# Performance work log

Hardware: AMD Instinct MI355X
Metric: run time of the kernel (lower is better)

## Reference

```python
import math
import jax, jax.numpy as jnp
import numpy as np

B, C, P, D = 4, 128, 128, 128  # note: C must equal D (see channel-branch einsum)
H = 8
R = D // H
G = 512
LN_EPS = 1e-5
L1_EPS = 1e-6


def layer_norm(x, g, b):
    m = x.mean(-1, keepdims=True)
    v = x.var(-1, keepdims=True)
    return (x - m) * jax.lax.rsqrt(v + LN_EPS) * g + b


def setup_inputs() -> dict:
    key = jax.random.key(0)
    ks = jax.random.split(key, 8)
    return {
        "qz": jax.random.normal(ks[0], (B, C, P, D), jnp.float32),
        "unary": jax.random.normal(ks[1], (B, C, P, D), jnp.float32),
        "time_u_weight": jax.random.normal(ks[2], (B, D, D), jnp.float32) * 0.05,
        "time_v_weight": jax.random.normal(ks[3], (B, D, D), jnp.float32) * 0.05,
        "channel_u_weight": jax.random.normal(ks[4], (B, D, D), jnp.float32) * 0.05,
        "channel_v_weight": jax.random.normal(ks[5], (B, D, D), jnp.float32) * 0.05,
        "topic_binary": jax.random.normal(ks[6], (B, G, D), jnp.float32) * 0.05,
        "ln_gamma": jnp.ones((D,), jnp.float32),
        "ln_beta": jnp.zeros((D,), jnp.float32),
        "w1": jax.random.normal(ks[7], (D, D), jnp.float32) * (1.0 / math.sqrt(D)),
        "b1": jnp.zeros((D,), jnp.float32),
        "w2": jax.random.normal(jax.random.fold_in(key, 99), (D, D), jnp.float32) * (1.0 / math.sqrt(D)),
        "b2": jnp.zeros((D,), jnp.float32),
    }


def reference(qz, unary, time_u_weight, time_v_weight, channel_u_weight,
              channel_v_weight, topic_binary, ln_gamma, ln_beta, w1, b1, w2, b2):
    old = qz
    qzn = layer_norm(qz, ln_gamma, ln_beta)
    scale = 1.0 / math.sqrt(R)

    def batched_linear(x, w):  # x: [B,C,P,D], w: [B,O,D] -> [B,C,P,O]
        return jnp.einsum('bcpd,bod->bcpo', x, w)

    # ---- time attention branch: attend over patches P per (channel, head) ----
    tu = batched_linear(qzn, time_u_weight).reshape(B, C, P, H, R).transpose(0, 1, 3, 2, 4)  # bchpr
    tv = batched_linear(qzn, time_v_weight).reshape(B, C, P, H, R).transpose(0, 1, 3, 2, 4)
    attn_t = jax.nn.softmax(jnp.einsum('bchpr,bchqr->bchpq', tu, tv) * scale, axis=-1)
    m_t = jnp.einsum('bchpq,bcqd->bchpd', attn_t, qzn).mean(axis=2)  # [B,C,P,D]

    # ---- channel attention branch: attend over channels C per (patch, head) ----
    cu = batched_linear(qzn, channel_u_weight).reshape(B, C, P, H, R).transpose(0, 2, 3, 1, 4)  # bphcr
    cv = batched_linear(qzn, channel_v_weight).reshape(B, C, P, H, R).transpose(0, 2, 3, 1, 4)
    attn_c = jax.nn.softmax(jnp.einsum('bphcr,bphdr->bphcd', cu, cv) * scale, axis=-1)
    qz_patch = qzn.transpose(0, 2, 1, 3)  # [B,P,C,D]; requires C == D
    m_c = (attn_c * qz_patch[:, :, None, :, :]).mean(axis=2).transpose(0, 2, 1, 3)  # [B,C,P,D]

    # ---- topic branch: relu + L1 normalize over topics ----
    qg = jnp.maximum(jnp.einsum('bcpd,bgd->bcpg', qzn, topic_binary), 0.0)
    qg = qg / jnp.clip(qg.sum(axis=-1, keepdims=True), L1_EPS, None)
    m_g = jnp.einsum('bcpg,bgd->bcpd', qg, topic_binary)

    x = 0.5 * (unary + m_t + m_c + m_g + old)
    h = layer_norm(x, ln_gamma, ln_beta)
    h = jax.nn.gelu(h @ w1.T + b1, approximate=False) @ w2.T + b2
    return x + h
```

## Files before the change

### kernel.cpp

```cpp
#include <hip/hip_runtime.h>

typedef __attribute__((ext_vector_type(8))) short short8;
typedef __attribute__((ext_vector_type(4))) float f32x4;
typedef unsigned short u16;
typedef unsigned int u32;

#define DEV static __device__ __forceinline__

constexpr long long NEL = 4LL * 128 * 128 * 128;

DEV float us2f(u16 u) { union { u32 i; float f; } x; x.i = (u32)u << 16; return x.f; }
DEV u16 f2us(float f) {
  union { float f; u32 i; } x; x.f = f;
  u32 r = x.i + 0x7fffu + ((x.i >> 16) & 1u);
  return (u16)(r >> 16);
}
DEV u32 pack2(float a, float b) { return (u32)f2us(a) | ((u32)f2us(b) << 16); }
DEV float gelu_f(float x) { return 0.5f * x * (1.0f + erff(x * 0.70710678118654752f)); }

__global__ __launch_bounds__(256) void ln_kernel(const float* __restrict__ xin,
                                                 const float* __restrict__ gw,
                                                 const float* __restrict__ bw,
                                                 u16* __restrict__ out) {
  int wv = threadIdx.x >> 6, lane = threadIdx.x & 63;
  long long row = (long long)blockIdx.x * 4 + wv;
  const float* xr = xin + row * 128;
  float2 v = *(const float2*)(xr + lane * 2);
  float a0 = v.x, a1 = v.y;
  float s = a0 + a1, q = a0 * a0 + a1 * a1;
  #pragma unroll
  for (int off = 32; off >= 1; off >>= 1) { s += __shfl_xor(s, off); q += __shfl_xor(q, off); }
  float m = s * (1.f / 128.f);
  float vv = q * (1.f / 128.f) - m * m;
  float r = rsqrtf(vv + 1e-5f);
  u32* orow = (u32*)(out + row * 128);
  orow[lane] = pack2((a0 - m) * r * gw[lane * 2] + bw[lane * 2],
                     (a1 - m) * r * gw[lane * 2 + 1] + bw[lane * 2 + 1]);
}

__global__ __launch_bounds__(256) void convert_weights(const float* __restrict__ t0, const float* __restrict__ t1,
                                                       const float* __restrict__ t2, const float* __restrict__ t3,
                                                       const float* __restrict__ w1, const float* __restrict__ w2,
                                                       u16* __restrict__ out) {
  long long e = ((long long)blockIdx.x * 256 + threadIdx.x) * 2;
  const float* src; long long off;
  if (e < 262144) {
    int t = (int)(e >> 16);
    src = t == 0 ? t0 : t == 1 ? t1 : t == 2 ? t2 : t3;
    off = e & 65535;
  } else if (e < 278528) { src = w1; off = e - 262144; }
  else { src = w2; off = e - 278528; }
  float2 v = *(const float2*)(src + off);
  *(u32*)(out + e) = pack2(v.x, v.y);
}

template <int EPI>
__global__ __launch_bounds__(256) void gemm128(const u16* __restrict__ A, const u16* __restrict__ W,
                                               int wbatched, const float* __restrict__ bias,
                                               const float* __restrict__ resid,
                                               float* __restrict__ outf, u16* __restrict__ outb) {
  __shared__ u16 AL[64][136];
  __shared__ u16 WL[128][136];
  int rowbase = blockIdx.x * 64;
  int bb = rowbase >> 14;
  const u32* Au = (const u32*)(A + (long long)rowbase * 128);
  const u32* Wu = (const u32*)(W + (wbatched ? (long long)bb * 16384 : 0));
  int tid = threadIdx.x, l = tid & 63, w = tid >> 6;
  for (int idx = tid; idx < 4096; idx += 256)
    *(u32*)&AL[idx >> 6][(idx & 63) * 2] = Au[idx];
  for (int idx = tid; idx < 8192; idx += 256)
    *(u32*)&WL[idx >> 6][(idx & 63) * 2] = Wu[idx];
  __syncthreads();
  f32x4 acc[8];
  #pragma unroll
  for (int cf = 0; cf < 8; ++cf) acc[cf] = (f32x4){0.f, 0.f, 0.f, 0.f};
  int arow = w * 16 + (l & 15);
  int kg = (l >> 4) * 8;
  #pragma unroll
  for (int k = 0; k < 4; ++k) {
    short8 a = *(const short8*)&AL[arow][k * 32 + kg];
    #pragma unroll
    for (int cf = 0; cf < 8; ++cf) {
      short8 b = *(const short8*)&WL[cf * 16 + (l & 15)][k * 32 + kg];
      acc[cf] = __builtin_amdgcn_mfma_f32_16x16x32_bf16(a, b, acc[cf], 0, 0, 0);
    }
  }
  #pragma unroll
  for (int cf = 0; cf < 8; ++cf) {
    int col = cf * 16 + (l & 15);
    float bv = 0.f;
    if (EPI == 2 || EPI == 3) bv = bias[col];
    #pragma unroll
    for (int j = 0; j < 4; ++j) {
      int row = rowbase + w * 16 + (l >> 4) * 4 + j;
      float v = acc[cf][j];
      if (EPI == 2) {
        outb[(long long)row * 128 + col] = f2us(gelu_f(v + bv));
      } else if (EPI == 3) {
        long long o = (long long)row * 128 + col;
        outf[o] = v + bv + resid[o];
      } else if (EPI == 4) {
        outb[(long long)row * 128 + col] = f2us(v);
      } else {
        int b2i = row >> 14, c = (row >> 7) & 127, p = row & 127;
        outb[((long long)(b2i * 128 + p) * 128 + c) * 128 + col] = f2us(v);
      }
    }
  }
}

__global__ __launch_bounds__(256) void time_attn(const u16* __restrict__ tu,
                                                 const u16* __restrict__ tv,
                                                 const u16* __restrict__ qzn16,
                                                 float* __restrict__ accg) {
  __shared__ u16 ZT[128][136];
  __shared__ u16 SP[4][32][136];
  int bc = blockIdx.x;
  const u16* ub = tu + (long long)bc * 16384;
  const u16* vb = tv + (long long)bc * 16384;
  const u32* zb32 = (const u32*)(qzn16 + (long long)bc * 16384);
  int tid = threadIdx.x, l = tid & 63, w = tid >> 6;
  int lo = l & 15, hi = l >> 4;
  int p0 = w * 32;
  for (int idx = tid; idx < 8192; idx += 256) {
    int dp = idx & 63, q = idx >> 6;
    u32 v = zb32[q * 64 + dp];
    ZT[2 * dp][q] = (u16)v;
    ZT[2 * dp + 1][q] = (u16)(v >> 16);
  }
  const short8 z8 = {0, 0, 0, 0, 0, 0, 0, 0};
  const f32x4 z4 = {0.f, 0.f, 0.f, 0.f};
  f32x4 ssum[2][8];
  #pragma unroll
  for (int i = 0; i < 2; ++i)
    #pragma unroll
    for (int cf = 0; cf < 8; ++cf) ssum[i][cf] = z4;
  bool act = hi < 2;
  for (int h = 0; h < 8; ++h) {
    int koff = h * 16 + hi * 8;
    short8 a[2];
    #pragma unroll
    for (int i = 0; i < 2; ++i)
      a[i] = act ? *(const short8*)(ub + (p0 + i * 16 + lo) * 128 + koff) : z8;
    f32x4 s[2][8];
    #pragma unroll
    for (int cf = 0; cf < 8; ++cf) {
      short8 bf = act ? *(const short8*)(vb + (cf * 16 + lo) * 128 + koff) : z8;
      #pragma unroll
      for (int i = 0; i < 2; ++i)
        s[i][cf] = __builtin_amdgcn_mfma_f32_16x16x32_bf16(a[i], bf, z4, 0, 0, 0);
    }
    float mx[2][4], rs[2][4];
    #pragma unroll
    for (int i = 0; i < 2; ++i)
      #pragma unroll
      for (int j = 0; j < 4; ++j) {
        float m = s[i][0][j];
        #pragma unroll
        for (int cf = 1; cf < 8; ++cf) m = fmaxf(m, s[i][cf][j]);
        #pragma unroll
        for (int off = 1; off <= 8; off <<= 1) m = fmaxf(m, __shfl_xor(m, off));
        mx[i][j] = m;
      }
    #pragma unroll
    for (int i = 0; i < 2; ++i)
      #pragma unroll
      for (int cf = 0; cf < 8; ++cf)
        #pragma unroll
        for (int j = 0; j < 4; ++j)
          s[i][cf][j] = __expf((s[i][cf][j] - mx[i][j]) * 0.25f);
    #pragma unroll
    for (int i = 0; i < 2; ++i)
      #pragma unroll
      for (int j = 0; j < 4; ++j) {
        float t = s[i][0][j];
        #pragma unroll
        for (int cf = 1; cf < 8; ++cf) t += s[i][cf][j];
        #pragma unroll
        for (int off = 1; off <= 8; off <<= 1) t += __shfl_xor(t, off);
        rs[i][j] = 1.f / t;
      }
    #pragma unroll
    for (int i = 0; i < 2; ++i)
      #pragma unroll
      for (int cf = 0; cf < 8; ++cf)
        #pragma unroll
        for (int j = 0; j < 4; ++j)
          ssum[i][cf][j] += s[i][cf][j] * rs[i][j];
  }
  #pragma unroll
  for (int i = 0; i < 2; ++i)
    #pragma unroll
    for (int cf = 0; cf < 8; ++cf)
      #pragma unroll
      for (int j = 0; j < 4; ++j)
        SP[w][i * 16 + hi * 4 + j][cf * 16 + lo] = f2us(ssum[i][cf][j]);
  __syncthreads();
  f32x4 acc[2][8];
  #pragma unroll
  for (int i = 0; i < 2; ++i)
    #pragma unroll
    for (int dt = 0; dt < 8; ++dt) acc[i][dt] = z4;
  #pragma unroll
  for (int kk = 0; kk < 4; ++kk) {
    short8 a[2];
    #pragma unroll
    for (int i = 0; i < 2; ++i)
      a[i] = *(const short8*)&SP[w][i * 16 + lo][kk * 32 + hi * 8];
    #pragma unroll
    for (int dt = 0; dt < 8; ++dt) {
      short8 bf = *(const short8*)&ZT[dt * 16 + lo][kk * 32 + hi * 8];
      #pragma unroll
      for (int i = 0; i < 2; ++i)
        acc[i][dt] = __builtin_amdgcn_mfma_f32_16x16x32_bf16(a[i], bf, acc[i][dt], 0, 0, 0);
    }
  }
  float* og = accg + (long long)bc * 16384;
  #pragma unroll
  for (int i = 0; i < 2; ++i)
    #pragma unroll
    for (int dt = 0; dt < 8; ++dt)
      #pragma unroll
      for (int j = 0; j < 4; ++j)
        og[(p0 + i * 16 + hi * 4 + j) * 128 + dt * 16 + lo] = acc[i][dt][j] * 0.125f;
}

__global__ __launch_bounds__(256) void chan_attn(const u16* __restrict__ cuT,
                                                 const u16* __restrict__ cvT,
                                                 const u16* __restrict__ qzn16,
                                                 float* __restrict__ accg) {
  int bp = blockIdx.x;
  int b = bp >> 7, p = bp & 127;
  const u16* ub = cuT + (long long)bp * 16384;
  const u16* vb = cvT + (long long)bp * 16384;
  int tid = threadIdx.x, l = tid & 63, w = tid >> 6;
  int lo = l & 15, hi = l >> 4;
  int c0 = w * 32;
  const short8 z8 = {0, 0, 0, 0, 0, 0, 0, 0};
  const f32x4 z4 = {0.f, 0.f, 0.f, 0.f};
  f32x4 ssum[2][8];
  #pragma unroll
  for (int i = 0; i < 2; ++i)
    #pragma unroll
    for (int cf = 0; cf < 8; ++cf) ssum[i][cf] = z4;
  bool act = hi < 2;
  for (int h = 0; h < 8; ++h) {
    int koff = h * 16 + hi * 8;
    short8 a[2];
    #pragma unroll
    for (int i = 0; i < 2; ++i)
      a[i] = act ? *(const short8*)(ub + (c0 + i * 16 + lo) * 128 + koff) : z8;
    f32x4 s[2][8];
    #pragma unroll
    for (int cf = 0; cf < 8; ++cf) {
      short8 bf = act ? *(const short8*)(vb + (cf * 16 + lo) * 128 + koff) : z8;
      #pragma unroll
      for (int i = 0; i < 2; ++i)
        s[i][cf] = __builtin_amdgcn_mfma_f32_16x16x32_bf16(a[i], bf, z4, 0, 0, 0);
    }
    float mx[2][4], rs[2][4];
    #pragma unroll
    for (int i = 0; i < 2; ++i)
      #pragma unroll
      for (int j = 0; j < 4; ++j) {
        float m = s[i][0][j];
        #pragma unroll
        for (int cf = 1; cf < 8; ++cf) m = fmaxf(m, s[i][cf][j]);
        #pragma unroll
        for (int off = 1; off <= 8; off <<= 1) m = fmaxf(m, __shfl_xor(m, off));
        mx[i][j] = m;
      }
    #pragma unroll
    for (int i = 0; i < 2; ++i)
      #pragma unroll
      for (int cf = 0; cf < 8; ++cf)
        #pragma unroll
        for (int j = 0; j < 4; ++j)
          s[i][cf][j] = __expf((s[i][cf][j] - mx[i][j]) * 0.25f);
    #pragma unroll
    for (int i = 0; i < 2; ++i)
      #pragma unroll
      for (int j = 0; j < 4; ++j) {
        float t = s[i][0][j];
        #pragma unroll
        for (int cf = 1; cf < 8; ++cf) t += s[i][cf][j];
        #pragma unroll
        for (int off = 1; off <= 8; off <<= 1) t += __shfl_xor(t, off);
        rs[i][j] = 1.f / t;
      }
    #pragma unroll
    for (int i = 0; i < 2; ++i)
      #pragma unroll
      for (int cf = 0; cf < 8; ++cf)
        #pragma unroll
        for (int j = 0; j < 4; ++j)
          ssum[i][cf][j] += s[i][cf][j] * rs[i][j];
  }
  const u16* zb = qzn16 + (long long)b * 2097152;
  float* ob = accg + (long long)b * 2097152;
  #pragma unroll
  for (int i = 0; i < 2; ++i)
    #pragma unroll
    for (int cf = 0; cf < 8; ++cf)
      #pragma unroll
      for (int j = 0; j < 4; ++j) {
        int c = c0 + i * 16 + hi * 4 + j;
        int o = cf * 16 + lo;
        long long off = ((long long)c * 128 + p) * 128 + o;
        ob[off] += ssum[i][cf][j] * 0.125f * us2f(zb[off]);
      }
}

__global__ __launch_bounds__(256) void topic_transpose(const float* __restrict__ topic,
                                                       u16* __restrict__ topicB, u16* __restrict__ topicT) {
  __shared__ u16 tile[64][136];
  int b = blockIdx.x >> 3, gc = blockIdx.x & 7;
  const float* tb = topic + (long long)b * 65536;
  u16* tBo = topicB + (long long)b * 65536;
  for (int idx = threadIdx.x; idx < 64 * 64; idx += 256) {
    int g = idx >> 6, d2 = idx & 63;
    const float2 v = *(const float2*)(tb + (long long)(gc * 64 + g) * 128 + d2 * 2);
    u32 pv = pack2(v.x, v.y);
    *(u32*)&tile[g][d2 * 2] = pv;
    *(u32*)(tBo + (long long)(gc * 64 + g) * 128 + d2 * 2) = pv;
  }
  __syncthreads();
  u16* to = topicT + (long long)b * 65536;
  for (int idx = threadIdx.x; idx < 128 * 64; idx += 256) {
    int d = idx >> 6, g = idx & 63;
    to[d * 512 + gc * 64 + g] = tile[g][d];
  }
}

__global__ __launch_bounds__(256) void topic_kernel(const u16* __restrict__ qzn16,
                                                    const u16* __restrict__ topicB,
                                                    const u16* __restrict__ topicT,
                                                    float* __restrict__ accg) {
  __shared__ u16 AL[32][136];
  __shared__ u16 QG[32][520];
  __shared__ float redsum[4][32];
  int rowbase = blockIdx.x * 32;
  int b = rowbase >> 14;
  const u16* tB = topicB + (long long)b * 65536;
  const u16* tT = topicT + (long long)b * 65536;
  int tid = threadIdx.x, l = tid & 63, w = tid >> 6;
  int lo = l & 15, hi = l >> 4;
  const u32* asrc = (const u32*)(qzn16 + (long long)rowbase * 128);
  for (int idx = tid; idx < 2048; idx += 256)
    *(u32*)&AL[idx >> 6][(idx & 63) * 2] = asrc[idx];
  __syncthreads();
  const f32x4 z4 = {0.f, 0.f, 0.f, 0.f};
  float rsum[2][4] = {{0.f,0.f,0.f,0.f},{0.f,0.f,0.f,0.f}};
  #pragma unroll
  for (int gc = 0; gc < 8; ++gc) {
    f32x4 pa[2] = {z4, z4};
    #pragma unroll
    for (int k = 0; k < 4; ++k) {
      short8 bb = *(const short8*)(tB + (long long)(gc * 64 + w * 16 + lo) * 128 + k * 32 + hi * 8);
      #pragma unroll
      for (int i = 0; i < 2; ++i) {
        short8 a = *(const short8*)&AL[i * 16 + lo][k * 32 + hi * 8];
        pa[i] = __builtin_amdgcn_mfma_f32_16x16x32_bf16(a, bb, pa[i], 0, 0, 0);
      }
    }
    #pragma unroll
    for (int i = 0; i < 2; ++i)
      #pragma unroll
      for (int j = 0; j < 4; ++j) {
        float v = fmaxf(pa[i][j], 0.f);
        QG[i * 16 + hi * 4 + j][gc * 64 + w * 16 + lo] = f2us(v);
        rsum[i][j] += v;
      }
  }
  #pragma unroll
  for (int i = 0; i < 2; ++i)
    #pragma unroll
    for (int j = 0; j < 4; ++j) {
      float t = rsum[i][j];
      #pragma unroll
      for (int off = 1; off <= 8; off <<= 1) t += __shfl_xor(t, off);
      rsum[i][j] = t;
    }
  if (lo == 0) {
    #pragma unroll
    for (int i = 0; i < 2; ++i)
      #pragma unroll
      for (int j = 0; j < 4; ++j)
        redsum[w][i * 16 + hi * 4 + j] = rsum[i][j];
  }
  __syncthreads();
  float inv[2][4];
  #pragma unroll
  for (int i = 0; i < 2; ++i)
    #pragma unroll
    for (int j = 0; j < 4; ++j) {
      int row = i * 16 + hi * 4 + j;
      float s = redsum[0][row] + redsum[1][row] + redsum[2][row] + redsum[3][row];
      inv[i][j] = 1.f / fmaxf(s, 1e-6f);
    }
  f32x4 ba[2][2] = {{z4, z4}, {z4, z4}};
  #pragma unroll
  for (int kc = 0; kc < 16; ++kc) {
    short8 a[2];
    #pragma unroll
    for (int i = 0; i < 2; ++i)
      a[i] = *(const short8*)&QG[i * 16 + lo][kc * 32 + hi * 8];
    #pragma unroll
    for (int cf = 0; cf < 2; ++cf) {
      short8 bb = *(const short8*)(tT + (long long)(w * 32 + cf * 16 + lo) * 512 + kc * 32 + hi * 8);
      #pragma unroll
      for (int i = 0; i < 2; ++i)
        ba[i][cf] = __builtin_amdgcn_mfma_f32_16x16x32_bf16(a[i], bb, ba[i][cf], 0, 0, 0);
    }
  }
  #pragma unroll
  for (int i = 0; i < 2; ++i)
    #pragma unroll
    for (int cf = 0; cf < 2; ++cf)
      #pragma unroll
      for (int j = 0; j < 4; ++j) {
        long long o = (long long)(rowbase + i * 16 + hi * 4 + j) * 128 + w * 32 + cf * 16 + lo;
        accg[o] += ba[i][cf][j] * inv[i][j];
      }
}

__global__ __launch_bounds__(256) void combine_kernel(const float* __restrict__ qz, const float* __restrict__ un,
                                                      float* __restrict__ acc) {
  long long i = ((long long)blockIdx.x * 256 + threadIdx.x) * 4;
  float4 q = *(const float4*)(qz + i);
  float4 u = *(const float4*)(un + i);
  float4 a = *(const float4*)(acc + i);
  float4 r;
  r.x = 0.5f * (q.x + u.x + a.x);
  r.y = 0.5f * (q.y + u.y + a.y);
  r.z = 0.5f * (q.z + u.z + a.z);
  r.w = 0.5f * (q.w + u.w + a.w);
  *(float4*)(acc + i) = r;
}

extern "C" void kernel_launch(void* const* d_in, const int* in_sizes, int n_in,
                              void* d_out, int out_size, void* d_ws, size_t ws_size,
                              hipStream_t stream) {
  const float* qz    = (const float*)d_in[0];
  const float* unary = (const float*)d_in[1];
  const float* tuw   = (const float*)d_in[2];
  const float* tvw   = (const float*)d_in[3];
  const float* cuw   = (const float*)d_in[4];
  const float* cvw   = (const float*)d_in[5];
  const float* topic = (const float*)d_in[6];
  const float* gam   = (const float*)d_in[7];
  const float* bet   = (const float*)d_in[8];
  const float* w1    = (const float*)d_in[9];
  const float* b1    = (const float*)d_in[10];
  const float* w2    = (const float*)d_in[11];
  const float* b2    = (const float*)d_in[12];
  float* out = (float*)d_out;

  char* base = (char*)d_ws;
  u16*   qzn16  = (u16*)base;
  float* accb   = (float*)(base + NEL * 2);
  u16*   bufU16 = (u16*)(base + NEL * 6);
  u16*   bufV16 = (u16*)(base + NEL * 8);
  u16*   wbf    = (u16*)(base + NEL * 10);
  u16*   topicB = wbf + 294912;
  u16*   topicT = topicB + 262144;

  convert_weights<<<576, 256, 0, stream>>>(tuw, tvw, cuw, cvw, w1, w2, wbf);
  topic_transpose<<<32, 256, 0, stream>>>(topic, topicB, topicT);
  ln_kernel<<<16384, 256, 0, stream>>>(qz, gam, bet, qzn16);
  gemm128<4><<<1024, 256, 0, stream>>>(qzn16, wbf,         1, nullptr, nullptr, nullptr, bufU16);
  gemm128<4><<<1024, 256, 0, stream>>>(qzn16, wbf + 65536, 1, nullptr, nullptr, nullptr, bufV16);
  time_attn<<<512, 256, 0, stream>>>(bufU16, bufV16, qzn16, accb);
  gemm128<5><<<1024, 256, 0, stream>>>(qzn16, wbf + 131072, 1, nullptr, nullptr, nullptr, bufU16);
  gemm128<5><<<1024, 256, 0, stream>>>(qzn16, wbf + 196608, 1, nullptr, nullptr, nullptr, bufV16);
  chan_attn<<<512, 256, 0, stream>>>(bufU16, bufV16, qzn16, accb);
  topic_kernel<<<2048, 256, 0, stream>>>(qzn16, topicB, topicT, accb);
  combine_kernel<<<8192, 256, 0, stream>>>(qz, unary, accb);
  ln_kernel<<<16384, 256, 0, stream>>>(accb, gam, bet, bufU16);
  gemm128<2><<<1024, 256, 0, stream>>>(bufU16, wbf + 262144, 0, b1, nullptr, nullptr, bufV16);
  gemm128<3><<<1024, 256, 0, stream>>>(bufV16, wbf + 278528, 0, b2, accb, out, nullptr);
}
```

Baseline: 395.7 us.

## Fuse dual projection GEMMs, stage V in LDS, fold combine+LN into topic kernel

Merges each pair of U/V projection GEMMs into one kernel that loads the activation tile once and reuses it for both weight matrices. The time and channel attention kernels now stage the V tile in shared memory instead of reading it repeatedly from global memory; time_attn reuses that buffer for the softmax scratch. The topic kernel now also does the residual combine and the second layer norm, which removes the separate combine and LN launches and their full-tensor round trips. The fused LN computes variance as E[x^2]-m^2, which is less numerically stable, and the extra shared memory may lower occupancy.

Result: no change. 394.3 us (-0.4%).

```diff
diff --git a/kernel.cpp b/kernel.cpp
--- a/kernel.cpp
+++ b/kernel.cpp
@@ -56,15 +56,14 @@
 
 template <int EPI>
 __global__ __launch_bounds__(256) void gemm128(const u16* __restrict__ A, const u16* __restrict__ W,
-                                               int wbatched, const float* __restrict__ bias,
+                                               const float* __restrict__ bias,
                                                const float* __restrict__ resid,
                                                float* __restrict__ outf, u16* __restrict__ outb) {
   __shared__ u16 AL[64][136];
   __shared__ u16 WL[128][136];
   int rowbase = blockIdx.x * 64;
-  int bb = rowbase >> 14;
   const u32* Au = (const u32*)(A + (long long)rowbase * 128);
-  const u32* Wu = (const u32*)(W + (wbatched ? (long long)bb * 16384 : 0));
+  const u32* Wu = (const u32*)W;
   int tid = threadIdx.x, l = tid & 63, w = tid >> 6;
   for (int idx = tid; idx < 4096; idx += 256)
     *(u32*)&AL[idx >> 6][(idx & 63) * 2] = Au[idx];
@@ -88,24 +87,70 @@
   #pragma unroll
   for (int cf = 0; cf < 8; ++cf) {
     int col = cf * 16 + (l & 15);
-    float bv = 0.f;
-    if (EPI == 2 || EPI == 3) bv = bias[col];
+    float bv = bias[col];
     #pragma unroll
     for (int j = 0; j < 4; ++j) {
       int row = rowbase + w * 16 + (l >> 4) * 4 + j;
       float v = acc[cf][j];
       if (EPI == 2) {
         outb[(long long)row * 128 + col] = f2us(gelu_f(v + bv));
-      } else if (EPI == 3) {
+      } else {
         long long o = (long long)row * 128 + col;
         outf[o] = v + bv + resid[o];
-      } else if (EPI == 4) {
-        outb[(long long)row * 128 + col] = f2us(v);
-      } else {
-        int b2i = row >> 14, c = (row >> 7) & 127, p = row & 127;
-        outb[((long long)(b2i * 128 + p) * 128 + c) * 128 + col] = f2us(v);
-      }
-    }
+      }
+    }
+  }
+}
+
+template <int EPI>
+__global__ __launch_bounds__(256) void gemm_dual(const u16* __restrict__ A,
+                                                 const u16* __restrict__ W0, const u16* __restrict__ W1,
+                                                 u16* __restrict__ out0, u16* __restrict__ out1) {
+  __shared__ u16 AL[64][136];
+  __shared__ u16 WL[128][136];
+  int rowbase = blockIdx.x * 64;
+  int bb = rowbase >> 14;
+  const u32* Au = (const u32*)(A + (long long)rowbase * 128);
+  int tid = threadIdx.x, l = tid & 63, w = tid >> 6;
+  for (int idx = tid; idx < 4096; idx += 256)
+    *(u32*)&AL[idx >> 6][(idx & 63) * 2] = Au[idx];
+  int arow = w * 16 + (l & 15);
+  int kg = (l >> 4) * 8;
+  #pragma unroll
+  for (int widx = 0; widx < 2; ++widx) {
+    const u32* Wu = (const u32*)((widx ? W1 : W0) + (long long)bb * 16384);
+    for (int idx = tid; idx < 8192; idx += 256)
+      *(u32*)&WL[idx >> 6][(idx & 63) * 2] = Wu[idx];
+    __syncthreads();
+    f32x4 acc[8];
+    #pragma unroll
+    for (int cf = 0; cf < 8; ++cf) acc[cf] = (f32x4){0.f, 0.f, 0.f, 0.f};
+    #pragma unroll
+    for (int k = 0; k < 4; ++k) {
+      short8 a = *(const short8*)&AL[arow][k * 32 + kg];
+      #pragma unroll
+      for (int cf = 0; cf < 8; ++cf) {
+        short8 b = *(const short8*)&WL[cf * 16 + (l & 15)][k * 32 + kg];
+        acc[cf] = __builtin_amdgcn_mfma_f32_16x16x32_bf16(a, b, acc[cf], 0, 0, 0);
+      }
+    }
+    u16* ob = widx ? out1 : out0;
+    #pragma unroll
+    for (int cf = 0; cf < 8; ++cf) {
+      int col = cf * 16 + (l & 15);
+      #pragma unroll
+      for (int j = 0; j < 4; ++j) {
+        int row = rowbase + w * 16 + (l >> 4) * 4 + j;
+        float v = acc[cf][j];
+        if (EPI == 4) {
+          ob[(long long)row * 128 + col] = f2us(v);
+        } else {
+          int b2i = row >> 14, c = (row >> 7) & 127, p = row & 127;
+          ob[((long long)(b2i * 128 + p) * 128 + c) * 128 + col] = f2us(v);
+        }
+      }
+    }
+    __syncthreads();
   }
 }
 
@@ -114,20 +159,25 @@
                                                  const u16* __restrict__ qzn16,
                                                  float* __restrict__ accg) {
   __shared__ u16 ZT[128][136];
-  __shared__ u16 SP[4][32][136];
+  __shared__ u16 UB[17408];
+  #define VB_(r, c) UB[(r) * 136 + (c)]
+  #define SP_(wv, r, c) UB[((wv) * 32 + (r)) * 136 + (c)]
   int bc = blockIdx.x;
   const u16* ub = tu + (long long)bc * 16384;
-  const u16* vb = tv + (long long)bc * 16384;
+  const u32* vb32 = (const u32*)(tv + (long long)bc * 16384);
   const u32* zb32 = (const u32*)(qzn16 + (long long)bc * 16384);
   int tid = threadIdx.x, l = tid & 63, w = tid >> 6;
   int lo = l & 15, hi = l >> 4;
   int p0 = w * 32;
   for (int idx = tid; idx < 8192; idx += 256) {
     int dp = idx & 63, q = idx >> 6;
-    u32 v = zb32[q * 64 + dp];
+    u32 v = zb32[idx];
     ZT[2 * dp][q] = (u16)v;
     ZT[2 * dp + 1][q] = (u16)(v >> 16);
   }
+  for (int idx = tid; idx < 8192; idx += 256)
+    *(u32*)&VB_(idx >> 6, (idx & 63) * 2) = vb32[idx];
+  __syncthreads();
   const short8 z8 = {0, 0, 0, 0, 0, 0, 0, 0};
   const f32x4 z4 = {0.f, 0.f, 0.f, 0.f};
   f32x4 ssum[2][8];
@@ -145,7 +195,7 @@
     f32x4 s[2][8];
     #pragma unroll
     for (int cf = 0; cf < 8; ++cf) {
-      short8 bf = act ? *(const short8*)(vb + (cf * 16 + lo) * 128 + koff) : z8;
+      short8 bf = act ? *(const short8*)&VB_(cf * 16 + lo, koff) : z8;
       #pragma unroll
       for (int i = 0; i < 2; ++i)
         s[i][cf] = __builtin_amdgcn_mfma_f32_16x16x32_bf16(a[i], bf, z4, 0, 0, 0);
@@ -188,13 +238,14 @@
         for (int j = 0; j < 4; ++j)
           ssum[i][cf][j] += s[i][cf][j] * rs[i][j];
   }
+  __syncthreads();
   #pragma unroll
   for (int i = 0; i < 2; ++i)
     #pragma unroll
     for (int cf = 0; cf < 8; ++cf)
       #pragma unroll
       for (int j = 0; j < 4; ++j)
-        SP[w][i * 16 + hi * 4 + j][cf * 16 + lo] = f2us(ssum[i][cf][j]);
+        SP_(w, i * 16 + hi * 4 + j, cf * 16 + lo) = f2us(ssum[i][cf][j]);
   __syncthreads();
   f32x4 acc[2][8];
   #pragma unroll
@@ -206,7 +257,7 @@
     short8 a[2];
     #pragma unroll
     for (int i = 0; i < 2; ++i)
-      a[i] = *(const short8*)&SP[w][i * 16 + lo][kk * 32 + hi * 8];
+      a[i] = *(const short8*)&SP_(w, i * 16 + lo, kk * 32 + hi * 8);
     #pragma unroll
     for (int dt = 0; dt < 8; ++dt) {
       short8 bf = *(const short8*)&ZT[dt * 16 + lo][kk * 32 + hi * 8];
@@ -223,19 +274,25 @@
       #pragma unroll
       for (int j = 0; j < 4; ++j)
         og[(p0 + i * 16 + hi * 4 + j) * 128 + dt * 16 + lo] = acc[i][dt][j] * 0.125f;
+  #undef VB_
+  #undef SP_
 }
 
 __global__ __launch_bounds__(256) void chan_attn(const u16* __restrict__ cuT,
                                                  const u16* __restrict__ cvT,
                                                  const u16* __restrict__ qzn16,
                                                  float* __restrict__ accg) {
+  __shared__ u16 VB[128][136];
   int bp = blockIdx.x;
   int b = bp >> 7, p = bp & 127;
   const u16* ub = cuT + (long long)bp * 16384;
-  const u16* vb = cvT + (long long)bp * 16384;
+  const u32* vb32 = (const u32*)(cvT + (long long)bp * 16384);
   int tid = threadIdx.x, l = tid & 63, w = tid >> 6;
   int lo = l & 15, hi = l >> 4;
   int c0 = w * 32;
+  for (int idx = tid; idx < 8192; idx += 256)
+    *(u32*)&VB[idx >> 6][(idx & 63) * 2] = vb32[idx];
+  __syncthreads();
   const short8 z8 = {0, 0, 0, 0, 0, 0, 0, 0};
   const f32x4 z4 = {0.f, 0.f, 0.f, 0.f};
   f32x4 ssum[2][8];
@@ -253,7 +310,7 @@
     f32x4 s[2][8];
     #pragma unroll
     for (int cf = 0; cf < 8; ++cf) {
-      short8 bf = act ? *(const short8*)(vb + (cf * 16 + lo) * 128 + koff) : z8;
+      short8 bf = act ? *(const short8*)&VB[cf * 16 + lo][koff] : z8;
       #pragma unroll
       for (int i = 0; i < 2; ++i)
         s[i][cf] = __builtin_amdgcn_mfma_f32_16x16x32_bf16(a[i], bf, z4, 0, 0, 0);
@@ -332,13 +389,20 @@
   }
 }
 
-__global__ __launch_bounds__(256) void topic_kernel(const u16* __restrict__ qzn16,
-                                                    const u16* __restrict__ topicB,
-                                                    const u16* __restrict__ topicT,
-                                                    float* __restrict__ accg) {
+__global__ __launch_bounds__(256) void topic_fuse(const u16* __restrict__ qzn16,
+                                                  const u16* __restrict__ topicB,
+                                                  const u16* __restrict__ topicT,
+                                                  const float* __restrict__ qz,
+                                                  const float* __restrict__ un,
+                                                  const float* __restrict__ gam,
+                                                  const float* __restrict__ bet,
+                                                  float* __restrict__ accg,
+                                                  u16* __restrict__ xln) {
   __shared__ u16 AL[32][136];
   __shared__ u16 QG[32][520];
-  __shared__ float redsum[4][32];
+  __shared__ float redL[4][32];
+  __shared__ float redS[4][32];
+  __shared__ float redQ[4][32];
   int rowbase = blockIdx.x * 32;
   int b = rowbase >> 14;
   const u16* tB = topicB + (long long)b * 65536;
@@ -350,7 +414,7 @@
     *(u32*)&AL[idx >> 6][(idx & 63) * 2] = asrc[idx];
   __syncthreads();
   const f32x4 z4 = {0.f, 0.f, 0.f, 0.f};
-  float rsum[2][4] = {{0.f,0.f,0.f,0.f},{0.f,0.f,0.f,0.f}};
+  float rsum[2][4] = {{0.f, 0.f, 0.f, 0.f}, {0.f, 0.f, 0.f, 0.f}};
   #pragma unroll
   for (int gc = 0; gc < 8; ++gc) {
     f32x4 pa[2] = {z4, z4};
@@ -386,7 +450,7 @@
     for (int i = 0; i < 2; ++i)
       #pragma unroll
       for (int j = 0; j < 4; ++j)
-        redsum[w][i * 16 + hi * 4 + j] = rsum[i][j];
+        redL[w][i * 16 + hi * 4 + j] = rsum[i][j];
   }
   __syncthreads();
   float inv[2][4];
@@ -395,7 +459,7 @@
     #pragma unroll
     for (int j = 0; j < 4; ++j) {
       int row = i * 16 + hi * 4 + j;
-      float s = redsum[0][row] + redsum[1][row] + redsum[2][row] + redsum[3][row];
+      float s = redL[0][row] + redL[1][row] + redL[2][row] + redL[3][row];
       inv[i][j] = 1.f / fmaxf(s, 1e-6f);
     }
   f32x4 ba[2][2] = {{z4, z4}, {z4, z4}};
@@ -413,6 +477,14 @@
         ba[i][cf] = __builtin_amdgcn_mfma_f32_16x16x32_bf16(a[i], bb, ba[i][cf], 0, 0, 0);
     }
   }
+  float gv[2], bv[2];
+  #pragma unroll
+  for (int cf = 0; cf < 2; ++cf) {
+    int col = w * 32 + cf * 16 + lo;
+    gv[cf] = gam[col];
+    bv[cf] = bet[col];
+  }
+  float xv[2][2][4];
   #pragma unroll
   for (int i = 0; i < 2; ++i)
     #pragma unroll
@@ -420,22 +492,40 @@
       #pragma unroll
       for (int j = 0; j < 4; ++j) {
         long long o = (long long)(rowbase + i * 16 + hi * 4 + j) * 128 + w * 32 + cf * 16 + lo;
-        accg[o] += ba[i][cf][j] * inv[i][j];
-      }
-}
-
-__global__ __launch_bounds__(256) void combine_kernel(const float* __restrict__ qz, const float* __restrict__ un,
-                                                      float* __restrict__ acc) {
-  long long i = ((long long)blockIdx.x * 256 + threadIdx.x) * 4;
-  float4 q = *(const float4*)(qz + i);
-  float4 u = *(const float4*)(un + i);
-  float4 a = *(const float4*)(acc + i);
-  float4 r;
-  r.x = 0.5f * (q.x + u.x + a.x);
-  r.y = 0.5f * (q.y + u.y + a.y);
-  r.z = 0.5f * (q.z + u.z + a.z);
-  r.w = 0.5f * (q.w + u.w + a.w);
-  *(float4*)(acc + i) = r;
+        float v = 0.5f * (qz[o] + un[o] + accg[o] + ba[i][cf][j] * inv[i][j]);
+        xv[i][cf][j] = v;
+        accg[o] = v;
+      }
+  #pragma unroll
+  for (int i = 0; i < 2; ++i)
+    #pragma unroll
+    for (int j = 0; j < 4; ++j) {
+      float ps = xv[i][0][j] + xv[i][1][j];
+      float pq = xv[i][0][j] * xv[i][0][j] + xv[i][1][j] * xv[i][1][j];
+      #pragma unroll
+      for (int off = 1; off <= 8; off <<= 1) { ps += __shfl_xor(ps, off); pq += __shfl_xor(pq, off); }
+      if (lo == 0) {
+        redS[w][i * 16 + hi * 4 + j] = ps;
+        redQ[w][i * 16 + hi * 4 + j] = pq;
+      }
+    }
+  __syncthreads();
+  #pragma unroll
+  for (int i = 0; i < 2; ++i)
+    #pragma unroll
+    for (int j = 0; j < 4; ++j) {
+      int row = i * 16 + hi * 4 + j;
+      float S = redS[0][row] + redS[1][row] + redS[2][row] + redS[3][row];
+      float Q = redQ[0][row] + redQ[1][row] + redQ[2][row] + redQ[3][row];
+      float m = S * (1.f / 128.f);
+      float var = Q * (1.f / 128.f) - m * m;
+      float r = rsqrtf(var + 1e-5f);
+      #pragma unroll
+      for (int cf = 0; cf < 2; ++cf) {
+        long long o = (long long)(rowbase + row) * 128 + w * 32 + cf * 16 + lo;
+        xln[o] = f2us((xv[i][cf][j] - m) * r * gv[cf] + bv[cf]);
+      }
+    }
 }
 
 extern "C" void kernel_launch(void* const* d_in, const int* in_sizes, int n_in,
@@ -468,15 +558,11 @@
   convert_weights<<<576, 256, 0, stream>>>(tuw, tvw, cuw, cvw, w1, w2, wbf);
   topic_transpose<<<32, 256, 0, stream>>>(topic, topicB, topicT);
   ln_kernel<<<16384, 256, 0, stream>>>(qz, gam, bet, qzn16);
-  gemm128<4><<<1024, 256, 0, stream>>>(qzn16, wbf,         1, nullptr, nullptr, nullptr, bufU16);
-  gemm128<4><<<1024, 256, 0, stream>>>(qzn16, wbf + 65536, 1, nullptr, nullptr, nullptr, bufV16);
+  gemm_dual<4><<<1024, 256, 0, stream>>>(qzn16, wbf, wbf + 65536, bufU16, bufV16);
   time_attn<<<512, 256, 0, stream>>>(bufU16, bufV16, qzn16, accb);
-  gemm128<5><<<1024, 256, 0, stream>>>(qzn16, wbf + 131072, 1, nullptr, nullptr, nullptr, bufU16);
-  gemm128<5><<<1024, 256, 0, stream>>>(qzn16, wbf + 196608, 1, nullptr, nullptr, nullptr, bufV16);
+  gemm_dual<5><<<1024, 256, 0, stream>>>(qzn16, wbf + 131072, wbf + 196608, bufU16, bufV16);
   chan_attn<<<512, 256, 0, stream>>>(bufU16, bufV16, qzn16, accb);
-  topic_kernel<<<2048, 256, 0, stream>>>(qzn16, topicB, topicT, accb);
-  combine_kernel<<<8192, 256, 0, stream>>>(qz, unary, accb);
-  ln_kernel<<<16384, 256, 0, stream>>>(accb, gam, bet, bufU16);
-  gemm128<2><<<1024, 256, 0, stream>>>(bufU16, wbf + 262144, 0, b1, nullptr, nullptr, bufV16);
-  gemm128<3><<<1024, 256, 0, stream>>>(bufV16, wbf + 278528, 0, b2, accb, out, nullptr);
-}
+  topic_fuse<<<2048, 256, 0, stream>>>(qzn16, topicB, topicT, qz, unary, gam, bet, accb, bufU16);
+  gemm128<2><<<1024, 256, 0, stream>>>(bufU16, wbf + 262144, b1, nullptr, nullptr, bufV16);
+  gemm128<3><<<1024, 256, 0, stream>>>(bufV16, wbf + 278528, b2, accb, out, nullptr);
+}
```
